# Optimization experiments

Measured on AMD Instinct MI355X. Metric: run time of the kernel, lower is better.

Reference implementation:

```python
import jax, jax.numpy as jnp
import numpy as np

ALPHA = 0.2
NEG_BIG = -9e15

def setup_inputs() -> dict:
    key = jax.random.key(0)
    k1, k2, k3, k4 = jax.random.split(key, 4)
    B, N, F = 8, 2048, 256
    h = jax.random.normal(k1, (B, N, F), dtype=jnp.float32)
    adj = jax.random.randint(k2, (B, N, N), 0, 2, dtype=jnp.int32)
    W = jax.random.normal(k3, (F, F), dtype=jnp.float32) * (1.414 / jnp.sqrt(F))
    a = jax.random.normal(k4, (2 * F, 1), dtype=jnp.float32) * 0.1
    return {"h": h, "adj": adj, "W": W, "a": a}

def reference(h, adj, W, a):
    F_out = W.shape[1]
    Wh = jnp.einsum('bnf,fo->bno', h, W)            # [B,N,F]
    Wh1 = Wh @ a[:F_out]                             # [B,N,1]
    Wh2 = Wh @ a[F_out:]                             # [B,N,1]
    e = jax.nn.leaky_relu(Wh1 + jnp.swapaxes(Wh2, 1, 2), negative_slope=ALPHA)  # [B,N,N]
    scores = jnp.where(adj > 0, e, NEG_BIG)
    attention = jax.nn.softmax(scores, axis=-1)      # [B,N,N]
    h_prime = jnp.einsum('bnm,bmf->bnf', attention, Wh)
    out = h + jax.nn.elu(h_prime)                    # concat=True -> elu; residual add
    return (out, attention)
```

## Files before the change

kernel.cpp:

```cpp
#include <hip/hip_runtime.h>

#define NB 8
#define NN 2048
#define NF 256

typedef __attribute__((ext_vector_type(8))) short bf16x8;
typedef __attribute__((ext_vector_type(4))) float f32x4;

__device__ __forceinline__ unsigned short f2bf(float x) {
  union { float f; unsigned int i; } c; c.f = x;
  unsigned int r = c.i + 0x7FFFu + ((c.i >> 16) & 1u);
  return (unsigned short)(r >> 16);
}
__device__ __forceinline__ unsigned short f2bf_fast(float x) {
  union { float f; unsigned int i; } c; c.f = x;
  return (unsigned short)((c.i + 0x8000u) >> 16);
}
__device__ __forceinline__ bf16x8 cvt8(float4 c0, float4 c1) {
  union { bf16x8 v8; unsigned short us[8]; } cu;
  cu.us[0] = f2bf_fast(c0.x); cu.us[1] = f2bf_fast(c0.y);
  cu.us[2] = f2bf_fast(c0.z); cu.us[3] = f2bf_fast(c0.w);
  cu.us[4] = f2bf_fast(c1.x); cu.us[5] = f2bf_fast(c1.y);
  cu.us[6] = f2bf_fast(c1.z); cu.us[7] = f2bf_fast(c1.w);
  return cu.v8;
}

__global__ __launch_bounds__(256) void k_prep(
    const float* __restrict__ W, const float* __restrict__ a,
    unsigned short* __restrict__ WT, float* __restrict__ u, float* __restrict__ v) {
  int t = threadIdx.x;
  if (blockIdx.x < 256) {
    int k = blockIdx.x;
    WT[t * 256 + k] = f2bf(W[k * 256 + t]);
  } else {
    float su = 0.f, sv = 0.f;
    for (int o = 0; o < 256; ++o) {
      float w = W[t * 256 + o];
      su += w * a[o];
      sv += w * a[256 + o];
    }
    u[t] = su; v[t] = sv;
  }
}

__global__ __launch_bounds__(256) void k_wht(
    const float* __restrict__ h, const unsigned short* __restrict__ WTr,
    unsigned short* __restrict__ WhT) {
  int bx = blockIdx.x;
  int b = bx >> 6;
  int t = bx & 63;
  int fBlk = (t >> 4) * 64;
  int iBlk = (t & 15) * 128;
  int wave = threadIdx.x >> 6, lane = threadIdx.x & 63;
  int fW = fBlk + (wave >> 1) * 32;
  int iW = iBlk + (wave & 1) * 64;
  int l15 = lane & 15, q8 = (lane >> 4) * 8;
  const float* hB = h + (size_t)b * NN * NF;

  f32x4 acc[2][4];
#pragma unroll
  for (int mt = 0; mt < 2; ++mt)
#pragma unroll
    for (int nt = 0; nt < 4; ++nt)
      acc[mt][nt] = (f32x4){0.f, 0.f, 0.f, 0.f};

  for (int k0 = 0; k0 < NF; k0 += 32) {
    int kk = k0 + q8;
    bf16x8 af[2], bfr[4];
#pragma unroll
    for (int mt = 0; mt < 2; ++mt) {
      int f = fW + mt * 16 + l15;
      af[mt] = *(const bf16x8*)(WTr + f * 256 + kk);
    }
#pragma unroll
    for (int nt = 0; nt < 4; ++nt) {
      int i = iW + nt * 16 + l15;
      const float* p = hB + (size_t)i * NF + kk;
      bfr[nt] = cvt8(*(const float4*)p, *(const float4*)(p + 4));
    }
#pragma unroll
    for (int mt = 0; mt < 2; ++mt)
#pragma unroll
      for (int nt = 0; nt < 4; ++nt)
        acc[mt][nt] = __builtin_amdgcn_mfma_f32_16x16x32_bf16(af[mt], bfr[nt], acc[mt][nt], 0, 0, 0);
  }

  unsigned short* WhTb = WhT + (size_t)b * NF * NN;
  int q4 = (lane >> 4) * 4;
#pragma unroll
  for (int mt = 0; mt < 2; ++mt)
#pragma unroll
    for (int nt = 0; nt < 4; ++nt)
#pragma unroll
      for (int r = 0; r < 4; ++r) {
        int f = fW + mt * 16 + q4 + r;
        int i = iW + nt * 16 + l15;
        WhTb[(size_t)f * NN + i] = f2bf(acc[mt][nt][r]);
      }
}

__global__ __launch_bounds__(256) void k_proj(
    const float* __restrict__ h, const float* __restrict__ u,
    const float* __restrict__ v, float* __restrict__ Wh1, float* __restrict__ Wh2) {
  int row = blockIdx.x * 4 + (threadIdx.x >> 6);
  int lane = threadIdx.x & 63;
  float4 hv = *(const float4*)(h + (size_t)row * NF + lane * 4);
  const float* up = u + lane * 4;
  const float* vp = v + lane * 4;
  float su = hv.x * up[0] + hv.y * up[1] + hv.z * up[2] + hv.w * up[3];
  float sv = hv.x * vp[0] + hv.y * vp[1] + hv.z * vp[2] + hv.w * vp[3];
#pragma unroll
  for (int off = 32; off >= 1; off >>= 1) {
    su += __shfl_xor(su, off);
    sv += __shfl_xor(sv, off);
  }
  if (lane == 0) { Wh1[row] = su; Wh2[row] = sv; }
}

__global__ __launch_bounds__(256) void k_soft(
    const int* __restrict__ adj, const float* __restrict__ Wh1,
    const float* __restrict__ Wh2, float* __restrict__ att) {
  const float NEGBIG = -9.0e15f;
  int row = blockIdx.x * 4 + (threadIdx.x >> 6);
  int lane = threadIdx.x & 63;
  int b = row >> 11;
  const float* w2 = Wh2 + (b << 11);
  const int* arow = adj + (size_t)row * NN;
  float w1 = Wh1[row];

  float x[32];
#pragma unroll
  for (int c = 0; c < 8; ++c) {
    int j = c * 256 + lane * 4;
    int4 av = *(const int4*)(arow + j);
    float4 pv = *(const float4*)(w2 + j);
    float t;
    t = w1 + pv.x; t = t >= 0.f ? t : 0.2f * t; x[c*4+0] = (av.x > 0) ? t : NEGBIG;
    t = w1 + pv.y; t = t >= 0.f ? t : 0.2f * t; x[c*4+1] = (av.y > 0) ? t : NEGBIG;
    t = w1 + pv.z; t = t >= 0.f ? t : 0.2f * t; x[c*4+2] = (av.z > 0) ? t : NEGBIG;
    t = w1 + pv.w; t = t >= 0.f ? t : 0.2f * t; x[c*4+3] = (av.w > 0) ? t : NEGBIG;
  }

  float m = x[0];
#pragma unroll
  for (int k = 1; k < 32; ++k) m = fmaxf(m, x[k]);
#pragma unroll
  for (int off = 32; off >= 1; off >>= 1) m = fmaxf(m, __shfl_xor(m, off));
  float sum = 0.f;
#pragma unroll
  for (int k = 0; k < 32; ++k) { x[k] = __expf(x[k] - m); sum += x[k]; }
#pragma unroll
  for (int off = 32; off >= 1; off >>= 1) sum += __shfl_xor(sum, off);
  float iv = 1.0f / sum;

  float* orow = att + (size_t)row * NN;
#pragma unroll
  for (int c = 0; c < 8; ++c) {
    int j = c * 256 + lane * 4;
    *(float4*)(orow + j) = make_float4(x[c*4+0] * iv, x[c*4+1] * iv,
                                       x[c*4+2] * iv, x[c*4+3] * iv);
  }
}

__global__ __launch_bounds__(512, 4) void k_pv(
    const float* __restrict__ attf, const unsigned short* __restrict__ WhT,
    const float* __restrict__ h, float* __restrict__ out) {
  __shared__ __align__(16) unsigned short satt[16 * 2048];
  int bx = blockIdx.x;
  int b = bx >> 7;
  int i0 = (bx & 127) * 16;
  int tid = threadIdx.x;

  {
    int r = tid >> 5;
    int m0 = (tid & 31) * 8;
    const float* arow = attf + ((size_t)(b * NN + i0 + r)) * NN;
    unsigned short* srow = satt + r * 2048;
    int swz = r * 8;
#pragma unroll
    for (int c = 0; c < 8; ++c) {
      int j = c * 256 + m0;
      float4 p0 = *(const float4*)(arow + j);
      float4 p1 = *(const float4*)(arow + j + 4);
      *(bf16x8*)(srow + (j ^ swz)) = cvt8(p0, p1);
    }
  }
  __syncthreads();

  int wave = tid >> 6, lane = tid & 63;
  int fW = wave * 32;
  int l15 = lane & 15, q8 = (lane >> 4) * 8;
  const unsigned short* WTb = WhT + (size_t)b * NF * NN;
  const unsigned short* aRow = satt + l15 * 2048;
  int swzA = l15 * 8;

  f32x4 acc[2];
#pragma unroll
  for (int nt = 0; nt < 2; ++nt) acc[nt] = (f32x4){0.f, 0.f, 0.f, 0.f};

  for (int kk = 0; kk < NN; kk += 32) {
    bf16x8 afr = *(const bf16x8*)(aRow + (((kk + q8) ^ swzA)));
    bf16x8 bfr[2];
#pragma unroll
    for (int nt = 0; nt < 2; ++nt) {
      int f = fW + nt * 16 + l15;
      bfr[nt] = *(const bf16x8*)(WTb + (size_t)f * NN + kk + q8);
    }
#pragma unroll
    for (int nt = 0; nt < 2; ++nt)
      acc[nt] = __builtin_amdgcn_mfma_f32_16x16x32_bf16(afr, bfr[nt], acc[nt], 0, 0, 0);
  }

  int q4 = (lane >> 4) * 4;
#pragma unroll
  for (int nt = 0; nt < 2; ++nt)
#pragma unroll
    for (int r = 0; r < 4; ++r) {
      int i = i0 + q4 + r;
      int f = fW + nt * 16 + l15;
      size_t idx = ((size_t)(b * NN + i)) * NF + f;
      float hp = acc[nt][r];
      float el = hp > 0.f ? hp : expm1f(hp);
      out[idx] = h[idx] + el;
    }
}

extern "C" void kernel_launch(void* const* d_in, const int* in_sizes, int n_in,
                              void* d_out, int out_size, void* d_ws, size_t ws_size,
                              hipStream_t stream) {
  const float* h = nullptr; const int* adj = nullptr;
  const float* W = nullptr; const float* a = nullptr;
  for (int i = 0; i < n_in; ++i) {
    int s = in_sizes[i];
    if (s == NB * NN * NF) h = (const float*)d_in[i];
    else if (s == NB * NN * NN) adj = (const int*)d_in[i];
    else if (s == NF * NF) W = (const float*)d_in[i];
    else if (s == 2 * NF) a = (const float*)d_in[i];
  }

  float* out = (float*)d_out;
  float* att = out + (size_t)NB * NN * NF;

  char* ws = (char*)d_ws;
  unsigned short* WhT = (unsigned short*)ws;
  unsigned short* WTr = (unsigned short*)(ws + 8388608);
  float* u   = (float*)(ws + 8388608 + 131072);
  float* v   = u + 256;
  float* Wh1 = v + 256;
  float* Wh2 = Wh1 + NB * NN;

  k_prep<<<257, 256, 0, stream>>>(W, a, WTr, u, v);
  k_wht<<<512, 256, 0, stream>>>(h, WTr, WhT);
  k_proj<<<NB * NN / 4, 256, 0, stream>>>(h, u, v, Wh1, Wh2);
  k_soft<<<NB * NN / 4, 256, 0, stream>>>(adj, Wh1, Wh2, att);
  k_pv<<<NB * 128, 512, 0, stream>>>(att, WhT, h, out);
}
```

Measured before the change: 426.6 us.

## Software-pipeline WhT loads in k_pv and remap blocks across batches for XCD locality

The k_pv main loop becomes a 4-stage register prefetch pipeline: B fragments for the next 128 K columns are loaded while the MFMAs for the current ones run, and A fragments from shared memory are prefetched one step ahead. Block indices are also permuted so consecutive hardware block IDs (round-robin across XCDs) map to the same batch, improving L2 reuse of the WhT slice. This raises register pressure and adds branchy prefetch guards.

```diff
diff --git a/kernel.cpp b/kernel.cpp
--- a/kernel.cpp
+++ b/kernel.cpp
@@ -167,6 +167,7 @@
     const float* __restrict__ h, float* __restrict__ out) {
   __shared__ __align__(16) unsigned short satt[16 * 2048];
   int bx = blockIdx.x;
+  bx = (bx & 7) * 128 + (bx >> 3);
   int b = bx >> 7;
   int i0 = (bx & 127) * 16;
   int tid = threadIdx.x;
@@ -193,22 +194,65 @@
   const unsigned short* WTb = WhT + (size_t)b * NF * NN;
   const unsigned short* aRow = satt + l15 * 2048;
   int swzA = l15 * 8;
+  const unsigned short* bp = WTb + (size_t)(fW + l15) * NN + q8;
+  const size_t ROW16 = (size_t)16 * NN;
 
   f32x4 acc[2];
-#pragma unroll
-  for (int nt = 0; nt < 2; ++nt) acc[nt] = (f32x4){0.f, 0.f, 0.f, 0.f};
-
-  for (int kk = 0; kk < NN; kk += 32) {
-    bf16x8 afr = *(const bf16x8*)(aRow + (((kk + q8) ^ swzA)));
-    bf16x8 bfr[2];
-#pragma unroll
-    for (int nt = 0; nt < 2; ++nt) {
-      int f = fW + nt * 16 + l15;
-      bfr[nt] = *(const bf16x8*)(WTb + (size_t)f * NN + kk + q8);
-    }
-#pragma unroll
-    for (int nt = 0; nt < 2; ++nt)
-      acc[nt] = __builtin_amdgcn_mfma_f32_16x16x32_bf16(afr, bfr[nt], acc[nt], 0, 0, 0);
+  acc[0] = (f32x4){0.f, 0.f, 0.f, 0.f};
+  acc[1] = (f32x4){0.f, 0.f, 0.f, 0.f};
+
+  bf16x8 bb0[2], bb1[2], bb2[2], bb3[2];
+  bb0[0] = *(const bf16x8*)(bp + 0);    bb0[1] = *(const bf16x8*)(bp + ROW16 + 0);
+  bb1[0] = *(const bf16x8*)(bp + 32);   bb1[1] = *(const bf16x8*)(bp + ROW16 + 32);
+  bb2[0] = *(const bf16x8*)(bp + 64);   bb2[1] = *(const bf16x8*)(bp + ROW16 + 64);
+  bb3[0] = *(const bf16x8*)(bp + 96);   bb3[1] = *(const bf16x8*)(bp + ROW16 + 96);
+  bf16x8 a0 = *(const bf16x8*)(aRow + ((0 + q8) ^ swzA));
+  bf16x8 a1, a2, a3;
+
+  for (int kk = 0; kk < NN; kk += 128) {
+    a1 = *(const bf16x8*)(aRow + (((kk + 32) + q8) ^ swzA));
+    acc[0] = __builtin_amdgcn_mfma_f32_16x16x32_bf16(a0, bb0[0], acc[0], 0, 0, 0);
+    acc[1] = __builtin_amdgcn_mfma_f32_16x16x32_bf16(a0, bb0[1], acc[1], 0, 0, 0);
+    {
+      int kp = kk + 128;
+      if (kp < NN) {
+        bb0[0] = *(const bf16x8*)(bp + kp);
+        bb0[1] = *(const bf16x8*)(bp + ROW16 + kp);
+      }
+    }
+    a2 = *(const bf16x8*)(aRow + (((kk + 64) + q8) ^ swzA));
+    acc[0] = __builtin_amdgcn_mfma_f32_16x16x32_bf16(a1, bb1[0], acc[0], 0, 0, 0);
+    acc[1] = __builtin_amdgcn_mfma_f32_16x16x32_bf16(a1, bb1[1], acc[1], 0, 0, 0);
+    {
+      int kp = kk + 160;
+      if (kp < NN) {
+        bb1[0] = *(const bf16x8*)(bp + kp);
+        bb1[1] = *(const bf16x8*)(bp + ROW16 + kp);
+      }
+    }
+    a3 = *(const bf16x8*)(aRow + (((kk + 96) + q8) ^ swzA));
+    acc[0] = __builtin_amdgcn_mfma_f32_16x16x32_bf16(a2, bb2[0], acc[0], 0, 0, 0);
+    acc[1] = __builtin_amdgcn_mfma_f32_16x16x32_bf16(a2, bb2[1], acc[1], 0, 0, 0);
+    {
+      int kp = kk + 192;
+      if (kp < NN) {
+        bb2[0] = *(const bf16x8*)(bp + kp);
+        bb2[1] = *(const bf16x8*)(bp + ROW16 + kp);
+      }
+    }
+    {
+      int ka = kk + 128;
+      if (ka < NN) a0 = *(const bf16x8*)(aRow + ((ka + q8) ^ swzA));
+    }
+    acc[0] = __builtin_amdgcn_mfma_f32_16x16x32_bf16(a3, bb3[0], acc[0], 0, 0, 0);
+    acc[1] = __builtin_amdgcn_mfma_f32_16x16x32_bf16(a3, bb3[1], acc[1], 0, 0, 0);
+    {
+      int kp = kk + 224;
+      if (kp < NN) {
+        bb3[0] = *(const bf16x8*)(bp + kp);
+        bb3[1] = *(const bf16x8*)(bp + ROW16 + kp);
+      }
+    }
   }
 
   int q4 = (lane >> 4) * 4;
```

Measured after the change: 421.5 us. About the same (-1.2%).

## Drop LDS staging in k_pv, load attention directly with wider per-wave tiles

Applied to the files above, without the earlier changes.

The k_pv kernel no longer stages a 16-row attention tile into shared memory with a barrier. Each wave now reads its fp32 attention fragment straight from global memory, converts it to bf16 in registers, and computes 64 features (4 MFMA tiles) instead of 32. Blocks shrink to 256 threads. The block index is swizzled so that concurrently scheduled blocks spread across batches. This removes the LDS write and barrier phase and lets loads overlap with MFMA, but it doubles global and L2 reads of the attention rows, since four waves now each re-read the same rows.

```diff
diff --git a/kernel.cpp b/kernel.cpp
--- a/kernel.cpp
+++ b/kernel.cpp
@@ -162,58 +162,42 @@
   }
 }
 
-__global__ __launch_bounds__(512, 4) void k_pv(
+__global__ __launch_bounds__(256, 6) void k_pv(
     const float* __restrict__ attf, const unsigned short* __restrict__ WhT,
     const float* __restrict__ h, float* __restrict__ out) {
-  __shared__ __align__(16) unsigned short satt[16 * 2048];
   int bx = blockIdx.x;
+  bx = (bx & 7) * 128 + (bx >> 3);
   int b = bx >> 7;
   int i0 = (bx & 127) * 16;
-  int tid = threadIdx.x;
-
-  {
-    int r = tid >> 5;
-    int m0 = (tid & 31) * 8;
-    const float* arow = attf + ((size_t)(b * NN + i0 + r)) * NN;
-    unsigned short* srow = satt + r * 2048;
-    int swz = r * 8;
-#pragma unroll
-    for (int c = 0; c < 8; ++c) {
-      int j = c * 256 + m0;
-      float4 p0 = *(const float4*)(arow + j);
-      float4 p1 = *(const float4*)(arow + j + 4);
-      *(bf16x8*)(srow + (j ^ swz)) = cvt8(p0, p1);
-    }
-  }
-  __syncthreads();
-
-  int wave = tid >> 6, lane = tid & 63;
-  int fW = wave * 32;
+  int wave = threadIdx.x >> 6, lane = threadIdx.x & 63;
+  int fW = wave * 64;
   int l15 = lane & 15, q8 = (lane >> 4) * 8;
-  const unsigned short* WTb = WhT + (size_t)b * NF * NN;
-  const unsigned short* aRow = satt + l15 * 2048;
-  int swzA = l15 * 8;
-
-  f32x4 acc[2];
-#pragma unroll
-  for (int nt = 0; nt < 2; ++nt) acc[nt] = (f32x4){0.f, 0.f, 0.f, 0.f};
-
+
+  const float* aBase = attf + ((size_t)(b * NN + i0 + l15)) * NN + q8;
+  const unsigned short* bp = WhT + (size_t)b * NF * NN + (size_t)(fW + l15) * NN + q8;
+  const size_t R16 = (size_t)16 * NN;
+
+  f32x4 acc[4];
+#pragma unroll
+  for (int nt = 0; nt < 4; ++nt) acc[nt] = (f32x4){0.f, 0.f, 0.f, 0.f};
+
+#pragma unroll 2
   for (int kk = 0; kk < NN; kk += 32) {
-    bf16x8 afr = *(const bf16x8*)(aRow + (((kk + q8) ^ swzA)));
-    bf16x8 bfr[2];
-#pragma unroll
-    for (int nt = 0; nt < 2; ++nt) {
-      int f = fW + nt * 16 + l15;
-      bfr[nt] = *(const bf16x8*)(WTb + (size_t)f * NN + kk + q8);
-    }
-#pragma unroll
-    for (int nt = 0; nt < 2; ++nt)
+    float4 p0 = *(const float4*)(aBase + kk);
+    float4 p1 = *(const float4*)(aBase + kk + 4);
+    bf16x8 bfr[4];
+#pragma unroll
+    for (int nt = 0; nt < 4; ++nt)
+      bfr[nt] = *(const bf16x8*)(bp + (size_t)nt * R16 + kk);
+    bf16x8 afr = cvt8(p0, p1);
+#pragma unroll
+    for (int nt = 0; nt < 4; ++nt)
       acc[nt] = __builtin_amdgcn_mfma_f32_16x16x32_bf16(afr, bfr[nt], acc[nt], 0, 0, 0);
   }
 
   int q4 = (lane >> 4) * 4;
 #pragma unroll
-  for (int nt = 0; nt < 2; ++nt)
+  for (int nt = 0; nt < 4; ++nt)
 #pragma unroll
     for (int r = 0; r < 4; ++r) {
       int i = i0 + q4 + r;
@@ -253,5 +237,5 @@
   k_wht<<<512, 256, 0, stream>>>(h, WTr, WhT);
   k_proj<<<NB * NN / 4, 256, 0, stream>>>(h, u, v, Wh1, Wh2);
   k_soft<<<NB * NN / 4, 256, 0, stream>>>(adj, Wh1, Wh2, att);
-  k_pv<<<NB * 128, 512, 0, stream>>>(att, WhT, h, out);
-}
+  k_pv<<<NB * 128, 256, 0, stream>>>(att, WhT, h, out);
+}
```

Result: slower. 474.7 us (+11.3%).
